# Performance work log

Measured on AMD Instinct MI355X. Metric: run time of the kernel, lower is better.

## Reference

```python
import jax, jax.numpy as jnp
import numpy as np

B, S, HID = 2, 2048, 2048
H, D = 16, 128
BASE = 10000.0
NEG = -1e9


def _rope_tables(seq_len, dim, dtype):
    inv_freq = 1.0 / (BASE ** (jnp.arange(0, dim, 2, dtype=jnp.float32) / dim))
    pos = jnp.arange(seq_len, dtype=jnp.float32)
    freqs = jnp.einsum('s,d->sd', pos, inv_freq)          # [S, D/2]
    emb = jnp.concatenate([freqs, freqs], axis=-1)        # [S, D]
    return jnp.cos(emb).astype(dtype), jnp.sin(emb).astype(dtype)


def _rotate_half(x):
    x1, x2 = jnp.split(x, 2, axis=-1)
    return jnp.concatenate([-x2, x1], axis=-1)


def setup_inputs() -> dict:
    key = jax.random.key(0)
    k1, k2, k3 = jax.random.split(key, 3)
    x = jax.random.normal(k1, (B, S, HID), dtype=jnp.float32)
    w_qkv = jax.random.normal(k2, (HID, 3 * HID), dtype=jnp.float32) * (HID ** -0.5)
    w_out = jax.random.normal(k3, (HID, HID), dtype=jnp.float32) * (HID ** -0.5)
    return {"x": x, "w_qkv": w_qkv, "w_out": w_out}


def reference(x, w_qkv, w_out):
    b, s, _ = x.shape
    qkv = x @ w_qkv                                        # [B, S, 3*HID]
    qkv = qkv.reshape(b, s, 3, H, D).transpose(2, 0, 3, 1, 4)  # [3, B, H, S, D]
    q, k, v = qkv[0], qkv[1], qkv[2]
    cos, sin = _rope_tables(s, D, x.dtype)                 # [S, D]
    cos = cos[None, None]
    sin = sin[None, None]
    q = q * cos + _rotate_half(q) * sin
    k = k * cos + _rotate_half(k) * sin
    scale = 1.0 / np.sqrt(D)
    scores = jnp.einsum('bhqd,bhkd->bhqk', q, k) * scale   # [B, H, S, S]
    causal = jnp.triu(jnp.ones((s, s), dtype=bool), k=1)
    scores = jnp.where(causal[None, None], NEG, scores)
    attn = jax.nn.softmax(scores, axis=-1)
    out = jnp.einsum('bhqk,bhkd->bhqd', attn, v)           # [B, H, S, D]
    out = out.transpose(0, 2, 1, 3).reshape(b, s, H * D)
    return out @ w_out
```

## Files before the change

kernel.cpp:

```cpp
#include <hip/hip_runtime.h>
#include <hip/hip_bf16.h>

#define S_LEN 2048
#define HID_DIM 2048
#define NH 16
#define HD 128
#define N3 6144

typedef __bf16 bf16x8 __attribute__((ext_vector_type(8)));
typedef float f32x4 __attribute__((ext_vector_type(4)));
typedef float f32x16 __attribute__((ext_vector_type(16)));

#define MFMA16(a, b, c) __builtin_amdgcn_mfma_f32_16x16x32_bf16(a, b, c, 0, 0, 0)
#define MFMA32(a, b, c) __builtin_amdgcn_mfma_f32_32x32x16_bf16(a, b, c, 0, 0, 0)

__device__ __forceinline__ unsigned short f2bf(float f) {
  union { float f; unsigned u; } v; v.f = f;
  return (unsigned short)((v.u + 0x7fffu + ((v.u >> 16) & 1u)) >> 16);
}
__device__ __forceinline__ float bf2f(unsigned short h) {
  union { unsigned u; float f; } v; v.u = ((unsigned)h) << 16; return v.f;
}
__device__ __forceinline__ unsigned packbf2(float lo, float hi) {
  union { __hip_bfloat162 h2; unsigned u; } cv;
  cv.h2 = __float22bfloat162_rn(make_float2(lo, hi));
  return cv.u;
}
__device__ __forceinline__ void store_c(float* p, float v) { *p = v; }
__device__ __forceinline__ void store_c(unsigned short* p, float v) { *p = f2bf(v); }

__device__ __forceinline__ void async16(const void* g, void* l) {
  __builtin_amdgcn_global_load_lds((const __attribute__((address_space(1))) unsigned int*)g,
                                   (__attribute__((address_space(3))) unsigned int*)l,
                                   16, 0, 0);
}

template <int N> __device__ __forceinline__ void vmcnt();
template <> __device__ __forceinline__ void vmcnt<0>() { asm volatile("s_waitcnt vmcnt(0)" ::: "memory"); }
template <> __device__ __forceinline__ void vmcnt<5>() { asm volatile("s_waitcnt vmcnt(5)" ::: "memory"); }

__global__ __launch_bounds__(256) void cast_bf16(const float4* __restrict__ src,
                                                 ushort4* __restrict__ dst) {
  int i = blockIdx.x * 256 + threadIdx.x;
  float4 v = src[i];
  ushort4 o;
  o.x = f2bf(v.x); o.y = f2bf(v.y); o.z = f2bf(v.z); o.w = f2bf(v.w);
  dst[i] = o;
}

__global__ __launch_bounds__(256) void transpose_cast(const float* __restrict__ src,
                                                      unsigned short* __restrict__ dst,
                                                      int R, int Ccols) {
  __shared__ float t[32][33];
  int ct = Ccols >> 5;
  int bx = blockIdx.x % ct, by = blockIdx.x / ct;
  int c0 = bx << 5, r0 = by << 5;
  int lx = threadIdx.x & 31, ly = threadIdx.x >> 5;
#pragma unroll
  for (int i = 0; i < 32; i += 8)
    t[ly + i][lx] = src[(long long)(r0 + ly + i) * Ccols + c0 + lx];
  __syncthreads();
#pragma unroll
  for (int i = 0; i < 32; i += 8)
    dst[(long long)(c0 + ly + i) * R + r0 + lx] = f2bf(t[lx][ly + i]);
}

__global__ __launch_bounds__(256) void rope_tables(float* __restrict__ cosT,
                                                   float* __restrict__ sinT) {
  int idx = blockIdx.x * 256 + threadIdx.x;
  int s = idx >> 6, i = idx & 63;
  float invf = powf(10000.0f, -(float)i * (1.0f / 64.0f));
  float a = (float)s * invf;
  cosT[idx] = cosf(a);
  sinT[idx] = sinf(a);
}

__global__ __launch_bounds__(512) void gemm_qkv(const unsigned short* __restrict__ A,
                                                const unsigned short* __restrict__ Bt,
                                                unsigned short* __restrict__ C,
                                                int Mdim, int Ndim, int Kdim) {
  constexpr int AEL = 256 * 64;
  constexpr int BEL = 192 * 64;
  constexpr int BUFE = AEL + BEL;
  __shared__ unsigned short smem[2 * BUFE];

  const int ntn = Ndim / 192;
  const int nwg = (Mdim >> 8) * ntn;
  int bid = blockIdx.x;
  bid = (bid & 7) * (nwg >> 3) + (bid >> 3);
  const int tm = (bid / ntn) << 8;
  const int tn = (bid % ntn) * 192;

  const int tid = threadIdx.x;
  const int w = tid >> 6, l = tid & 63;
  const int g = l >> 4, cc = l & 15;
  const int wm = w >> 2, wn = w & 3;

  const int srow = tid >> 3;
  const int schunk = (tid & 7) ^ (srow & 7);
  const unsigned short* gA = A + (long long)(tm + srow) * Kdim + schunk * 8;
  const unsigned short* gB = Bt + (long long)(tn + srow) * Kdim + schunk * 8;

  const int ch0 = ((g) ^ (cc & 7)) << 3;
  const int ch1 = ((4 + g) ^ (cc & 7)) << 3;

  f32x4 acc[8][3] = {};
  bf16x8 a[4][2], b[3][2];
  const int nk = Kdim >> 6;

#define ST_A(kt2, BUF, s) \
  async16(gA + (long long)(s) * 64 * Kdim + ((long long)(kt2) << 6), \
          smem + (BUF) * BUFE + (s) * 4096 + w * 512)
#define ST_B(kt2, BUF, s) \
  async16(gB + (long long)(s) * 64 * Kdim + ((long long)(kt2) << 6), \
          smem + (BUF) * BUFE + AEL + (s) * 4096 + w * 512)

#pragma unroll
  for (int s = 0; s < 4; ++s) ST_A(0, 0, s);
#pragma unroll
  for (int s = 0; s < 3; ++s) ST_B(0, 0, s);
  ST_A(1, 1, 0); ST_A(1, 1, 2);
  ST_B(1, 1, 0); ST_B(1, 1, 1); ST_B(1, 1, 2);
  vmcnt<5>();
  __builtin_amdgcn_s_barrier();

#define KSTEP(kt, BUF, OBUF)                                                      \
  {                                                                               \
    const unsigned short* Ab = smem + (BUF) * BUFE + wm * (128 * 64);             \
    const unsigned short* Bb = smem + (BUF) * BUFE + AEL + wn * (48 * 64);        \
      \
    _Pragma("unroll") for (int i = 0; i < 4; ++i) {                               \
      const int r = (i * 16 + cc) << 6;                                           \
      a[i][0] = *(const bf16x8*)(Ab + r + ch0);                                   \
      a[i][1] = *(const bf16x8*)(Ab + r + ch1);                                   \
    }                                                                             \
    _Pragma("unroll") for (int j = 0; j < 2; ++j) {                               \
      const int r = (j * 16 + cc) << 6;                                           \
      b[j][0] = *(const bf16x8*)(Bb + r + ch0);                                   \
      b[j][1] = *(const bf16x8*)(Bb + r + ch1);                                   \
    }                                                                             \
    if ((kt) + 1 < nk) { ST_A((kt) + 1, OBUF, 1); ST_A((kt) + 1, OBUF, 3); }      \
    __builtin_amdgcn_s_barrier();                                                 \
    __builtin_amdgcn_s_setprio(1);                                                \
    _Pragma("unroll") for (int i = 0; i < 4; ++i)                                 \
      _Pragma("unroll") for (int j = 0; j < 2; ++j) {                             \
        acc[i][j] = MFMA16(a[i][0], b[j][0], acc[i][j]);                          \
        acc[i][j] = MFMA16(a[i][1], b[j][1], acc[i][j]);                          \
      }                                                                           \
    __builtin_amdgcn_s_setprio(0);                                                \
    __builtin_amdgcn_s_barrier();                                                 \
                   \
    {                                                                             \
      const int r = (2 * 16 + cc) << 6;                                           \
      b[2][0] = *(const bf16x8*)(Bb + r + ch0);                                   \
      b[2][1] = *(const bf16x8*)(Bb + r + ch1);                                   \
    }                                                                             \
    if ((kt) + 2 < nk) { ST_A((kt) + 2, BUF, 0); ST_A((kt) + 2, BUF, 2); }        \
    __builtin_amdgcn_s_barrier();                                                 \
    __builtin_amdgcn_s_setprio(1);                                                \
    _Pragma("unroll") for (int i = 0; i < 4; ++i) {                               \
      acc[i][2] = MFMA16(a[i][0], b[2][0], acc[i][2]);                            \
      acc[i][2] = MFMA16(a[i][1], b[2][1], acc[i][2]);                            \
    }                                                                             \
    __builtin_amdgcn_s_setprio(0);                                                \
    __builtin_amdgcn_s_barrier();                                                 \
            \
    _Pragma("unroll") for (int i = 0; i < 4; ++i) {                               \
      const int r = ((64 + i * 16 + cc) << 6);                                    \
      a[i][0] = *(const bf16x8*)(Ab + r + ch0);                                   \
      a[i][1] = *(const bf16x8*)(Ab + r + ch1);                                   \
    }                                                                             \
    if ((kt) + 2 < nk) { ST_B((kt) + 2, BUF, 0); ST_B((kt) + 2, BUF, 1); }        \
    __builtin_amdgcn_s_barrier();                                                 \
    __builtin_amdgcn_s_setprio(1);                                                \
    _Pragma("unroll") for (int i = 0; i < 4; ++i)                                 \
      _Pragma("unroll") for (int j = 0; j < 2; ++j) {                             \
        acc[4 + i][j] = MFMA16(a[i][0], b[j][0], acc[4 + i][j]);                  \
        acc[4 + i][j] = MFMA16(a[i][1], b[j][1], acc[4 + i][j]);                  \
      }                                                                           \
    __builtin_amdgcn_s_setprio(0);                                                \
    __builtin_amdgcn_s_barrier();                                                 \
               \
    if ((kt) + 2 < nk) { ST_B((kt) + 2, BUF, 2); }                                \
    __builtin_amdgcn_s_barrier();                                                 \
    __builtin_amdgcn_s_setprio(1);                                                \
    _Pragma("unroll") for (int i = 0; i < 4; ++i) {                               \
      acc[4 + i][2] = MFMA16(a[i][0], b[2][0], acc[4 + i][2]);                    \
      acc[4 + i][2] = MFMA16(a[i][1], b[2][1], acc[4 + i][2]);                    \
    }                                                                             \
    __builtin_amdgcn_s_setprio(0);                                                \
    if ((kt) + 2 < nk) vmcnt<5>(); else vmcnt<0>();                               \
    __builtin_amdgcn_s_barrier();                                                 \
  }

  for (int kt = 0; kt < nk; kt += 2) {
    KSTEP(kt, 0, 1);
    KSTEP(kt + 1, 1, 0);
  }
#undef KSTEP
#undef ST_A
#undef ST_B

  const int crow0 = tm + wm * 128;
  const int ccol0 = tn + wn * 48;
#pragma unroll
  for (int mi = 0; mi < 8; ++mi)
#pragma unroll
    for (int j = 0; j < 3; ++j)
#pragma unroll
      for (int p = 0; p < 4; ++p) {
        int row = crow0 + ((mi >> 2) << 6) + ((mi & 3) << 4) + (g << 2) + p;
        int col = ccol0 + j * 16 + cc;
        store_c(&C[(long long)row * Ndim + col], acc[mi][j][p]);
      }
}

template <int BM, int BN, typename OutT>
__global__ __launch_bounds__(512) void gemm_pipe8(const unsigned short* __restrict__ A,
                                                  const unsigned short* __restrict__ Bt,
                                                  OutT* __restrict__ C,
                                                  int Mdim, int Ndim, int Kdim) {
  constexpr int WTM = BM / 2, WTN = BN / 4;
  constexpr int MREP = WTM / 16, NREP = WTN / 16;
  constexpr int AEL = BM * 64, BEL = BN * 64, BUFE = AEL + BEL;
  constexpr int AINST = BM / 64, BINST = BN / 64;
  constexpr int AHALF = BM / 128, BHALF = BN / 128;
  constexpr int VN = BN / 64 + BM / 128;
  __shared__ unsigned short smem[2 * BUFE];

  const int ntn = Ndim / BN;
  const int nwg = (Mdim / BM) * ntn;
  int bid = blockIdx.x;
  bid = (bid & 7) * (nwg >> 3) + (bid >> 3);
  const int tm = (bid / ntn) * BM;
  const int tn = (bid % ntn) * BN;

  const int tid = threadIdx.x;
  const int w = tid >> 6, l = tid & 63;
  const int g = l >> 4, cc = l & 15;
  const int wm = w >> 2, wn = w & 3;

  const int srow = tid >> 3;
  const int schunk = (tid & 7) ^ (srow & 7);
  const unsigned short* gA = A + (long long)(tm + srow) * Kdim + schunk * 8;
  const unsigned short* gB = Bt + (long long)(tn + srow) * Kdim + schunk * 8;

  const int ch0 = ((g) ^ (cc & 7)) << 3;
  const int ch1 = ((4 + g) ^ (cc & 7)) << 3;

  f32x4 acc[MREP][NREP] = {};
  bf16x8 a[MREP / 2][2], b[NREP][2];

  const int nk = Kdim >> 6;

#define STAGE_A(kt2, s) \
  async16(gA + (long long)(s) * 64 * Kdim + ((long long)(kt2) << 6), \
          smem + ((kt2) & 1) * BUFE + (s) * 4096 + w * 512)
#define STAGE_B(kt2, s) \
  async16(gB + (long long)(s) * 64 * Kdim + ((long long)(kt2) << 6), \
          smem + ((kt2) & 1) * BUFE + AEL + (s) * 4096 + w * 512)

#pragma unroll
  for (int s = 0; s < AINST; ++s) STAGE_A(0, s);
#pragma unroll
  for (int s = 0; s < BINST; ++s) STAGE_B(0, s);
#pragma unroll
  for (int s = 0; s < BINST; ++s) STAGE_B(1, s);
#pragma unroll
  for (int s = 0; s < AHALF; ++s) STAGE_A(1, s);
  vmcnt<VN>();
  __builtin_amdgcn_s_barrier();

  for (int kt = 0; kt < nk; ++kt) {
    const int buf = kt & 1;
    const unsigned short* Ab = smem + buf * BUFE + (wm * WTM) * 64;
    const unsigned short* Bb = smem + buf * BUFE + AEL + (wn * WTN) * 64;

#pragma unroll
    for (int i = 0; i < MREP / 2; ++i) {
      const int r = (i * 16 + cc) << 6;
      a[i][0] = *(const bf16x8*)(Ab + r + ch0);
      a[i][1] = *(const bf16x8*)(Ab + r + ch1);
    }
#pragma unroll
    for (int j = 0; j < NREP; ++j) {
      const int r = (j * 16 + cc) << 6;
      b[j][0] = *(const bf16x8*)(Bb + r + ch0);
      b[j][1] = *(const bf16x8*)(Bb + r + ch1);
    }
    if (kt + 1 < nk) {
#pragma unroll
      for (int s = AHALF; s < AINST; ++s) STAGE_A(kt + 1, s);
    }
    __builtin_amdgcn_s_barrier();
    __builtin_amdgcn_s_setprio(1);
#pragma unroll
    for (int i = 0; i < MREP / 2; ++i)
#pragma unroll
      for (int j = 0; j < NREP / 2; ++j) {
        acc[i][j] = MFMA16(a[i][0], b[j][0], acc[i][j]);
        acc[i][j] = MFMA16(a[i][1], b[j][1], acc[i][j]);
      }
    __builtin_amdgcn_s_setprio(0);
    __builtin_amdgcn_s_barrier();

    if (kt + 2 < nk) {
#pragma unroll
      for (int s = 0; s < BHALF; ++s) STAGE_B(kt + 2, s);
    }
    __builtin_amdgcn_s_barrier();
    __builtin_amdgcn_s_setprio(1);
#pragma unroll
    for (int i = 0; i < MREP / 2; ++i)
#pragma unroll
      for (int j = 0; j < NREP / 2; ++j) {
        f32x4& ac = acc[i][NREP / 2 + j];
        ac = MFMA16(a[i][0], b[NREP / 2 + j][0], ac);
        ac = MFMA16(a[i][1], b[NREP / 2 + j][1], ac);
      }
    __builtin_amdgcn_s_setprio(0);
    __builtin_amdgcn_s_barrier();

#pragma unroll
    for (int i = 0; i < MREP / 2; ++i) {
      const int r = ((WTM / 2) + i * 16 + cc) << 6;
      a[i][0] = *(const bf16x8*)(Ab + r + ch0);
      a[i][1] = *(const bf16x8*)(Ab + r + ch1);
    }
    if (kt + 2 < nk) {
#pragma unroll
      for (int s = BHALF; s < BINST; ++s) STAGE_B(kt + 2, s);
    }
    __builtin_amdgcn_s_barrier();
    __builtin_amdgcn_s_setprio(1);
#pragma unroll
    for (int i = 0; i < MREP / 2; ++i)
#pragma unroll
      for (int j = 0; j < NREP / 2; ++j) {
        f32x4& ac = acc[MREP / 2 + i][j];
        ac = MFMA16(a[i][0], b[j][0], ac);
        ac = MFMA16(a[i][1], b[j][1], ac);
      }
    __builtin_amdgcn_s_setprio(0);
    __builtin_amdgcn_s_barrier();

    if (kt + 2 < nk) {
#pragma unroll
      for (int s = 0; s < AHALF; ++s) STAGE_A(kt + 2, s);
    }
    __builtin_amdgcn_s_barrier();
    __builtin_amdgcn_s_setprio(1);
#pragma unroll
    for (int i = 0; i < MREP / 2; ++i)
#pragma unroll
      for (int j = 0; j < NREP / 2; ++j) {
        f32x4& ac = acc[MREP / 2 + i][NREP / 2 + j];
        ac = MFMA16(a[i][0], b[NREP / 2 + j][0], ac);
        ac = MFMA16(a[i][1], b[NREP / 2 + j][1], ac);
      }
    __builtin_amdgcn_s_setprio(0);
    if (kt + 2 < nk) vmcnt<VN>(); else vmcnt<0>();
    __builtin_amdgcn_s_barrier();
  }
#undef STAGE_A
#undef STAGE_B

  const int crow0 = tm + wm * WTM;
  const int ccol0 = tn + wn * WTN;
#pragma unroll
  for (int i = 0; i < MREP; ++i)
#pragma unroll
    for (int j = 0; j < NREP; ++j)
#pragma unroll
      for (int p = 0; p < 4; ++p) {
        int row = crow0 + i * 16 + (g << 2) + p;
        int col = ccol0 + j * 16 + cc;
        store_c(&C[(long long)row * Ndim + col], acc[i][j][p]);
      }
}

__global__ __launch_bounds__(256) void split_rope(const unsigned short* __restrict__ qkv,
                                                  const float* __restrict__ cosT,
                                                  const float* __restrict__ sinT,
                                                  unsigned short* __restrict__ Qb,
                                                  unsigned short* __restrict__ Kb,
                                                  unsigned short* __restrict__ Vt) {
  __shared__ unsigned short vtile[32][128];
  const int bid = blockIdx.x;
  const int st = bid & 63;
  const int h = (bid >> 6) & 15;
  const int b = bid >> 10;
  const int s0 = st << 5;
  const int t = threadIdx.x;
  const int d = t & 127;
  const int sl0 = t >> 7;
  const int dh = d & 63;
  const float sgn = (d < 64) ? -1.0f : 1.0f;
  const float qscale = 0.08838834764831845f;
#pragma unroll
  for (int it = 0; it < 16; ++it) {
    const int sl = sl0 + (it << 1);
    const int s = s0 + sl;
    const long long rb = ((long long)(b * S_LEN + s)) * N3 + h * HD;
    const float cv = cosT[(s << 6) + dh];
    const float sv = sinT[(s << 6) + dh];
    float qv = bf2f(qkv[rb + d]);
    float qo = bf2f(qkv[rb + (d ^ 64)]);
    float kv = bf2f(qkv[rb + HID_DIM + d]);
    float ko = bf2f(qkv[rb + HID_DIM + (d ^ 64)]);
    const long long ob = ((long long)((b * NH + h) * S_LEN + s)) * HD + d;
    Qb[ob] = f2bf((qv * cv + sgn * qo * sv) * qscale);
    Kb[ob] = f2bf(kv * cv + sgn * ko * sv);
    vtile[sl][d] = qkv[rb + 2 * HID_DIM + d];
  }
  __syncthreads();
  const int dr = t >> 1;
  const int sh = (t & 1) << 4;
  unsigned short tv[16];
#pragma unroll
  for (int j = 0; j < 16; ++j) tv[j] = vtile[sh + j][dr];
  uint4 u0, u1;
  u0.x = (unsigned)tv[0] | ((unsigned)tv[1] << 16);
  u0.y = (unsigned)tv[2] | ((unsigned)tv[3] << 16);
  u0.z = (unsigned)tv[4] | ((unsigned)tv[5] << 16);
  u0.w = (unsigned)tv[6] | ((unsigned)tv[7] << 16);
  u1.x = (unsigned)tv[8] | ((unsigned)tv[9] << 16);
  u1.y = (unsigned)tv[10] | ((unsigned)tv[11] << 16);
  u1.z = (unsigned)tv[12] | ((unsigned)tv[13] << 16);
  u1.w = (unsigned)tv[14] | ((unsigned)tv[15] << 16);
  const long long vb = ((long long)((b * NH + h) * HD + dr)) * S_LEN + s0 + sh;
  *(uint4*)(Vt + vb) = u0;
  *(uint4*)(Vt + vb + 8) = u1;
}

__global__ __launch_bounds__(256) void flash_attn(const unsigned short* __restrict__ Qg,
                                                  const unsigned short* __restrict__ Kg,
                                                  const unsigned short* __restrict__ Vt,
                                                  unsigned short* __restrict__ Ob) {
  __shared__ unsigned short smem[32768];
  const int id = blockIdx.x;
  const int bh = id & 31;
  const int qtr = (id >> 5) & 7;
  const int qt = (id >> 8) ? qtr : 15 - qtr;
  const int Q0 = qt << 7;
  const int b = bh >> 4, h = bh & 15;
  const long long base = (long long)bh * (S_LEN * HD);
  const int tid = threadIdx.x, w = tid >> 6, l = tid & 63;
  const int hi = l >> 5, q = l & 31;
  const int q0w = Q0 + (w << 5);
  const int g = l >> 4, c = l & 15;

  bf16x8 qf[8];
  {
    const unsigned short* qp = Qg + base + (long long)(q0w + q) * HD + (hi << 3);
#pragma unroll
    for (int s = 0; s < 8; ++s) qf[s] = *(const bf16x8*)(qp + (s << 4));
  }

  f32x16 oacc[4] = {};
  float m = -1e30f, lsum = 0.f;

  const int nt = (qt << 1) + 2;

  auto STAGE = [&](int kv0, int buf) {
    unsigned short* ks = smem + buf * 8192;
    unsigned short* vs = smem + 16384 + buf * 8192;
#pragma unroll
    for (int j = 0; j < 4; ++j) {
      int row = (w << 4) + (j << 2) + g;
      int chunk = c ^ (row & 7);
      async16(Kg + base + (long long)(kv0 + row) * HD + (chunk << 3),
              ks + (((w << 4) + (j << 2)) << 7));
    }
#pragma unroll
    for (int j = 0; j < 4; ++j) {
      int dr = (w << 5) + (j << 3) + (l >> 3);
      int chunk = (l & 7) ^ (dr & 7);
      async16(Vt + base + (long long)dr * S_LEN + kv0 + (chunk << 3),
              vs + (((w << 5) + (j << 3)) << 6));
    }
  };

  STAGE(0, 0);
  __syncthreads();

  int cur = 0;
  for (int t = 0; t < nt; ++t) {
    const int kv0 = t << 6;
    if (t + 1 < nt) STAGE((t + 1) << 6, cur ^ 1);

    if (kv0 < q0w + 32) {
      const unsigned short* ks = smem + cur * 8192;
      const unsigned short* vs = smem + 16384 + cur * 8192;

      f32x16 sa[2] = {};
#pragma unroll
      for (int h2 = 0; h2 < 2; ++h2) {
        const char* kb = (const char*)ks + (((h2 << 5) + q) << 8);
        const int r7 = q & 7;
#pragma unroll
        for (int s = 0; s < 8; ++s) {
          bf16x8 kf = *(const bf16x8*)(kb + ((((s << 1) + hi) ^ r7) << 4));
          sa[h2] = MFMA32(kf, qf[s], sa[h2]);
        }
      }

      if (kv0 + 63 > q0w) {
        const int qq = q0w + q;
#pragma unroll
        for (int h2 = 0; h2 < 2; ++h2)
#pragma unroll
          for (int j = 0; j < 16; ++j) {
            int kv = kv0 + (h2 << 5) + (j & 3) + ((j >> 2) << 3) + (hi << 2);
            if (kv > qq) sa[h2][j] = -1e30f;
          }
      }

      float tmax = -1e30f;
#pragma unroll
      for (int h2 = 0; h2 < 2; ++h2)
#pragma unroll
        for (int j = 0; j < 16; ++j) tmax = fmaxf(tmax, sa[h2][j]);
      tmax = fmaxf(tmax, __shfl_xor(tmax, 32));
      float mn = fmaxf(m, tmax);
      float fsc = __expf(m - mn);
      m = mn;
      float ps = 0.f;
#pragma unroll
      for (int h2 = 0; h2 < 2; ++h2)
#pragma unroll
        for (int j = 0; j < 16; ++j) {
          float pv = __expf(sa[h2][j] - mn);
          sa[h2][j] = pv;
          ps += pv;
        }
      ps += __shfl_xor(ps, 32);
      lsum = lsum * fsc + ps;
#pragma unroll
      for (int db = 0; db < 4; ++db)
#pragma unroll
        for (int j = 0; j < 16; ++j) oacc[db][j] *= fsc;

      unsigned up[2][8], wp[2][8];
#pragma unroll
      for (int h2 = 0; h2 < 2; ++h2)
#pragma unroll
        for (int k = 0; k < 8; ++k)
          up[h2][k] = packbf2(sa[h2][2 * k], sa[h2][2 * k + 1]);
#pragma unroll
      for (int h2 = 0; h2 < 2; ++h2)
#pragma unroll
        for (int k = 0; k < 8; ++k)
          wp[h2][k] = __shfl_xor((int)up[h2][k], 32);
      union Frag { unsigned u[4]; bf16x8 v; } pf[4];
#pragma unroll
      for (int s = 0; s < 4; ++s) {
        int h2 = s >> 1, q4 = (s & 1) << 2;
        pf[s].u[0] = hi ? wp[h2][q4 + 2] : up[h2][q4];
        pf[s].u[1] = hi ? wp[h2][q4 + 3] : up[h2][q4 + 1];
        pf[s].u[2] = hi ? up[h2][q4 + 2] : wp[h2][q4];
        pf[s].u[3] = hi ? up[h2][q4 + 3] : wp[h2][q4 + 1];
      }

#pragma unroll
      for (int db = 0; db < 4; ++db) {
        const char* vb = (const char*)vs + (((db << 5) + q) << 7);
        const int d7 = q & 7;
#pragma unroll
        for (int s = 0; s < 4; ++s) {
          bf16x8 vf = *(const bf16x8*)(vb + ((((s << 1) + hi) ^ d7) << 4));
          oacc[db] = MFMA32(vf, pf[s].v, oacc[db]);
        }
      }
    }

    __syncthreads();
    cur ^= 1;
  }

  const float rl = 1.0f / lsum;
#pragma unroll
  for (int db = 0; db < 4; ++db)
#pragma unroll
    for (int jg = 0; jg < 4; ++jg) {
      int d = (db << 5) + (jg << 3) + (hi << 2);
      unsigned v0 = packbf2(oacc[db][4 * jg] * rl, oacc[db][4 * jg + 1] * rl);
      unsigned v1 = packbf2(oacc[db][4 * jg + 2] * rl, oacc[db][4 * jg + 3] * rl);
      *(uint2*)(smem + (((w << 5) + q) << 7) + d) = make_uint2(v0, v1);
    }
  __syncthreads();
  {
    const int qr = tid >> 1;
    const int dh = (tid & 1) << 6;
    const uint4* src = (const uint4*)(smem + (qr << 7) + dh);
    uint4* dst = (uint4*)(Ob + (long long)((b << 11) + Q0 + qr) * HID_DIM + (h << 7) + dh);
#pragma unroll
    for (int cc2 = 0; cc2 < 8; ++cc2) dst[cc2] = src[cc2];
  }
}

extern "C" void kernel_launch(void* const* d_in, const int* in_sizes, int n_in,
                              void* d_out, int out_size, void* d_ws, size_t ws_size,
                              hipStream_t stream) {
  (void)in_sizes; (void)n_in; (void)out_size; (void)ws_size;
  const float* x = (const float*)d_in[0];
  const float* w_qkv = (const float*)d_in[1];
  const float* w_out = (const float*)d_in[2];
  float* out = (float*)d_out;
  char* ws = (char*)d_ws;

  unsigned short* xb    = (unsigned short*)(ws);
  unsigned short* wqkvT = (unsigned short*)(ws + 16777216);
  unsigned short* woutT = (unsigned short*)(ws + 41943040);
  unsigned short* qkv   = (unsigned short*)(ws + 50331648);
  unsigned short* Qb    = (unsigned short*)(ws + 100663296);
  unsigned short* Kb    = (unsigned short*)(ws + 117440512);
  unsigned short* Vt    = (unsigned short*)(ws + 134217728);
  float* cosT = (float*)(ws + 150994944);
  float* sinT = (float*)(ws + 151519232);
  unsigned short* Ob = qkv;

  cast_bf16<<<8192, 256, 0, stream>>>((const float4*)x, (ushort4*)xb);
  transpose_cast<<<12288, 256, 0, stream>>>(w_qkv, wqkvT, 2048, 6144);
  transpose_cast<<<4096, 256, 0, stream>>>(w_out, woutT, 2048, 2048);
  rope_tables<<<512, 256, 0, stream>>>(cosT, sinT);
  gemm_qkv<<<512, 512, 0, stream>>>(xb, wqkvT, qkv, 4096, 6144, 2048);
  split_rope<<<2048, 256, 0, stream>>>(qkv, cosT, sinT, Qb, Kb, Vt);
  flash_attn<<<512, 256, 0, stream>>>(Qb, Kb, Vt, Ob);
  gemm_pipe8<128, 256, float><<<256, 512, 0, stream>>>(Ob, woutT, out, 4096, 2048, 2048);
}
```

Before: 286.9 us.

## Split QKV GEMM into 256x256 tile kernel plus 128x256 kernel for remainder

Replaces the 256x192-tile QKV GEMM with a 256x256-tile kernel covering the first 4096 output columns, and a second launch of the existing 128x256 pipelined GEMM for the last 2048 columns. An ldc parameter lets both kernels write into slices of the same qkv buffer. Larger tiles raise arithmetic intensity and cut LDS/global traffic per FLOP. The cost is more registers (a 32-tile accumulator), an extra kernel launch, and 256 blocks per launch, which may not balance well across the CUs.

```diff
diff --git a/kernel.cpp b/kernel.cpp
--- a/kernel.cpp
+++ b/kernel.cpp
@@ -38,6 +38,7 @@
 template <int N> __device__ __forceinline__ void vmcnt();
 template <> __device__ __forceinline__ void vmcnt<0>() { asm volatile("s_waitcnt vmcnt(0)" ::: "memory"); }
 template <> __device__ __forceinline__ void vmcnt<5>() { asm volatile("s_waitcnt vmcnt(5)" ::: "memory"); }
+template <> __device__ __forceinline__ void vmcnt<6>() { asm volatile("s_waitcnt vmcnt(6)" ::: "memory"); }
 
 __global__ __launch_bounds__(256) void cast_bf16(const float4* __restrict__ src,
                                                  ushort4* __restrict__ dst) {
@@ -75,21 +76,19 @@
   sinT[idx] = sinf(a);
 }
 
-__global__ __launch_bounds__(512) void gemm_qkv(const unsigned short* __restrict__ A,
-                                                const unsigned short* __restrict__ Bt,
-                                                unsigned short* __restrict__ C,
-                                                int Mdim, int Ndim, int Kdim) {
-  constexpr int AEL = 256 * 64;
-  constexpr int BEL = 192 * 64;
-  constexpr int BUFE = AEL + BEL;
+__global__ __launch_bounds__(512) void gemm256(const unsigned short* __restrict__ A,
+                                               const unsigned short* __restrict__ Bt,
+                                               unsigned short* __restrict__ C,
+                                               int Mdim, int Ncols, int ldc, int Kdim) {
+  constexpr int AEL = 256 * 64, BUFE = 2 * AEL;
   __shared__ unsigned short smem[2 * BUFE];
 
-  const int ntn = Ndim / 192;
+  const int ntn = Ncols >> 8;
   const int nwg = (Mdim >> 8) * ntn;
   int bid = blockIdx.x;
   bid = (bid & 7) * (nwg >> 3) + (bid >> 3);
   const int tm = (bid / ntn) << 8;
-  const int tn = (bid % ntn) * 192;
+  const int tn = (bid % ntn) << 8;
 
   const int tid = threadIdx.x;
   const int w = tid >> 6, l = tid & 63;
@@ -104,8 +103,8 @@
   const int ch0 = ((g) ^ (cc & 7)) << 3;
   const int ch1 = ((4 + g) ^ (cc & 7)) << 3;
 
-  f32x4 acc[8][3] = {};
-  bf16x8 a[4][2], b[3][2];
+  f32x4 acc[8][4] = {};
+  bf16x8 a[4][2], b[4][2];
   const int nk = Kdim >> 6;
 
 #define ST_A(kt2, BUF, s) \
@@ -118,17 +117,17 @@
 #pragma unroll
   for (int s = 0; s < 4; ++s) ST_A(0, 0, s);
 #pragma unroll
-  for (int s = 0; s < 3; ++s) ST_B(0, 0, s);
+  for (int s = 0; s < 4; ++s) ST_B(0, 0, s);
   ST_A(1, 1, 0); ST_A(1, 1, 2);
-  ST_B(1, 1, 0); ST_B(1, 1, 1); ST_B(1, 1, 2);
-  vmcnt<5>();
+  ST_B(1, 1, 0); ST_B(1, 1, 1); ST_B(1, 1, 2); ST_B(1, 1, 3);
+  vmcnt<6>();
   __builtin_amdgcn_s_barrier();
 
 #define KSTEP(kt, BUF, OBUF)                                                      \
   {                                                                               \
     const unsigned short* Ab = smem + (BUF) * BUFE + wm * (128 * 64);             \
-    const unsigned short* Bb = smem + (BUF) * BUFE + AEL + wn * (48 * 64);        \
-      \
+    const unsigned short* Bb = smem + (BUF) * BUFE + AEL + wn * (64 * 64);        \
+                    \
     _Pragma("unroll") for (int i = 0; i < 4; ++i) {                               \
       const int r = (i * 16 + cc) << 6;                                           \
       a[i][0] = *(const bf16x8*)(Ab + r + ch0);                                   \
@@ -149,22 +148,23 @@
       }                                                                           \
     __builtin_amdgcn_s_setprio(0);                                                \
     __builtin_amdgcn_s_barrier();                                                 \
-                   \
-    {                                                                             \
-      const int r = (2 * 16 + cc) << 6;                                           \
-      b[2][0] = *(const bf16x8*)(Bb + r + ch0);                                   \
-      b[2][1] = *(const bf16x8*)(Bb + r + ch1);                                   \
+                                              \
+    _Pragma("unroll") for (int j = 0; j < 2; ++j) {                               \
+      const int r = ((2 + j) * 16 + cc) << 6;                                     \
+      b[2 + j][0] = *(const bf16x8*)(Bb + r + ch0);                               \
+      b[2 + j][1] = *(const bf16x8*)(Bb + r + ch1);                               \
     }                                                                             \
     if ((kt) + 2 < nk) { ST_A((kt) + 2, BUF, 0); ST_A((kt) + 2, BUF, 2); }        \
     __builtin_amdgcn_s_barrier();                                                 \
     __builtin_amdgcn_s_setprio(1);                                                \
-    _Pragma("unroll") for (int i = 0; i < 4; ++i) {                               \
-      acc[i][2] = MFMA16(a[i][0], b[2][0], acc[i][2]);                            \
-      acc[i][2] = MFMA16(a[i][1], b[2][1], acc[i][2]);                            \
-    }                                                                             \
+    _Pragma("unroll") for (int i = 0; i < 4; ++i)                                 \
+      _Pragma("unroll") for (int j = 0; j < 2; ++j) {                             \
+        acc[i][2 + j] = MFMA16(a[i][0], b[2 + j][0], acc[i][2 + j]);              \
+        acc[i][2 + j] = MFMA16(a[i][1], b[2 + j][1], acc[i][2 + j]);              \
+      }                                                                           \
     __builtin_amdgcn_s_setprio(0);                                                \
     __builtin_amdgcn_s_barrier();                                                 \
-            \
+                                              \
     _Pragma("unroll") for (int i = 0; i < 4; ++i) {                               \
       const int r = ((64 + i * 16 + cc) << 6);                                    \
       a[i][0] = *(const bf16x8*)(Ab + r + ch0);                                   \
@@ -180,16 +180,17 @@
       }                                                                           \
     __builtin_amdgcn_s_setprio(0);                                                \
     __builtin_amdgcn_s_barrier();                                                 \
-               \
-    if ((kt) + 2 < nk) { ST_B((kt) + 2, BUF, 2); }                                \
+                            \
+    if ((kt) + 2 < nk) { ST_B((kt) + 2, BUF, 2); ST_B((kt) + 2, BUF, 3); }        \
     __builtin_amdgcn_s_barrier();                                                 \
     __builtin_amdgcn_s_setprio(1);                                                \
-    _Pragma("unroll") for (int i = 0; i < 4; ++i) {                               \
-      acc[4 + i][2] = MFMA16(a[i][0], b[2][0], acc[4 + i][2]);                    \
-      acc[4 + i][2] = MFMA16(a[i][1], b[2][1], acc[4 + i][2]);                    \
-    }                                                                             \
+    _Pragma("unroll") for (int i = 0; i < 4; ++i)                                 \
+      _Pragma("unroll") for (int j = 0; j < 2; ++j) {                             \
+        acc[4 + i][2 + j] = MFMA16(a[i][0], b[2 + j][0], acc[4 + i][2 + j]);      \
+        acc[4 + i][2 + j] = MFMA16(a[i][1], b[2 + j][1], acc[4 + i][2 + j]);      \
+      }                                                                           \
     __builtin_amdgcn_s_setprio(0);                                                \
-    if ((kt) + 2 < nk) vmcnt<5>(); else vmcnt<0>();                               \
+    if ((kt) + 2 < nk) vmcnt<6>(); else vmcnt<0>();                               \
     __builtin_amdgcn_s_barrier();                                                 \
   }
 
@@ -202,16 +203,16 @@
 #undef ST_B
 
   const int crow0 = tm + wm * 128;
-  const int ccol0 = tn + wn * 48;
-#pragma unroll
-  for (int mi = 0; mi < 8; ++mi)
-#pragma unroll
-    for (int j = 0; j < 3; ++j)
+  const int ccol0 = tn + wn * 64;
+#pragma unroll
+  for (int i = 0; i < 8; ++i)
+#pragma unroll
+    for (int j = 0; j < 4; ++j)
 #pragma unroll
       for (int p = 0; p < 4; ++p) {
-        int row = crow0 + ((mi >> 2) << 6) + ((mi & 3) << 4) + (g << 2) + p;
+        int row = crow0 + i * 16 + (g << 2) + p;
         int col = ccol0 + j * 16 + cc;
-        store_c(&C[(long long)row * Ndim + col], acc[mi][j][p]);
+        store_c(&C[(long long)row * ldc + col], acc[i][j][p]);
       }
 }
 
@@ -219,7 +220,7 @@
 __global__ __launch_bounds__(512) void gemm_pipe8(const unsigned short* __restrict__ A,
                                                   const unsigned short* __restrict__ Bt,
                                                   OutT* __restrict__ C,
-                                                  int Mdim, int Ndim, int Kdim) {
+                                                  int Mdim, int Ncols, int ldc, int Kdim) {
   constexpr int WTM = BM / 2, WTN = BN / 4;
   constexpr int MREP = WTM / 16, NREP = WTN / 16;
   constexpr int AEL = BM * 64, BEL = BN * 64, BUFE = AEL + BEL;
@@ -228,7 +229,7 @@
   constexpr int VN = BN / 64 + BM / 128;
   __shared__ unsigned short smem[2 * BUFE];
 
-  const int ntn = Ndim / BN;
+  const int ntn = Ncols / BN;
   const int nwg = (Mdim / BM) * ntn;
   int bid = blockIdx.x;
   bid = (bid & 7) * (nwg >> 3) + (bid >> 3);
@@ -375,7 +376,7 @@
       for (int p = 0; p < 4; ++p) {
         int row = crow0 + i * 16 + (g << 2) + p;
         int col = ccol0 + j * 16 + cc;
-        store_c(&C[(long long)row * Ndim + col], acc[i][j][p]);
+        store_c(&C[(long long)row * ldc + col], acc[i][j][p]);
       }
 }
 
@@ -624,8 +625,10 @@
   transpose_cast<<<12288, 256, 0, stream>>>(w_qkv, wqkvT, 2048, 6144);
   transpose_cast<<<4096, 256, 0, stream>>>(w_out, woutT, 2048, 2048);
   rope_tables<<<512, 256, 0, stream>>>(cosT, sinT);
-  gemm_qkv<<<512, 512, 0, stream>>>(xb, wqkvT, qkv, 4096, 6144, 2048);
+  gemm256<<<256, 512, 0, stream>>>(xb, wqkvT, qkv, 4096, 4096, 6144, 2048);
+  gemm_pipe8<128, 256, unsigned short><<<256, 512, 0, stream>>>(
+      xb, wqkvT + (long long)4096 * 2048, qkv + 4096, 4096, 2048, 6144, 2048);
   split_rope<<<2048, 256, 0, stream>>>(qkv, cosT, sinT, Qb, Kb, Vt);
   flash_attn<<<512, 256, 0, stream>>>(Qb, Kb, Vt, Ob);
-  gemm_pipe8<128, 256, float><<<256, 512, 0, stream>>>(Ob, woutT, out, 4096, 2048, 2048);
-}
+  gemm_pipe8<128, 256, float><<<256, 512, 0, stream>>>(Ob, woutT, out, 4096, 2048, 2048, 2048);
+}
```

Result: no change. 281.5 us (-1.9%).
